# Performance work log

Hardware: AMD Instinct MI355X
Metric: run time of the kernel (lower is better)

Reference implementation:

```python
import jax, jax.numpy as jnp
import numpy as np
import math

SQRT2 = float(np.sqrt(2.0))
INV_SQRT_2PI = float(1.0 / np.sqrt(2.0 * np.pi))


def _trunc_prob(x, mu, sigma):
    # Faithful port of TruncNormal.prob with a=-10, b=10
    a, b = -10.0, 10.0
    phi_b = 0.5 * (1.0 + jax.scipy.special.erf((b - mu) / sigma / SQRT2))
    phi_a = 0.5 * (1.0 + jax.scipy.special.erf((a - mu) / sigma / SQRT2))
    xs = jnp.where(x > b, x + 100.0, x)
    xs = jnp.where(xs < a, xs - 100.0, xs)
    xn = (xs - mu) / sigma
    dens = jnp.exp(-0.5 * xn * xn) * INV_SQRT_2PI
    dens = jnp.where((xn > b) | (xn < a), 0.0, dens)
    return dens / (phi_b - phi_a) + 1e-10


def _S_single(zg, tt, Wx, bx, Wt, bt, Wt2, bt2, Wf, bf, Wo, bo):
    # One tiny MLP applied to one group-slice zg (shape [g]) at scalar time tt.
    g = Wx.shape[0]
    x = jnp.tanh(Wx @ zg + bx)
    half = g // 2
    freqs = jnp.exp(jnp.arange(half, dtype=zg.dtype) * (-math.log(10000.0) / half))
    te = tt * freqs
    temb = jnp.concatenate([jnp.sin(te), jnp.cos(te)])  # [g]
    tv = jax.nn.gelu(Wt @ temb + bt, approximate=False)  # torch nn.GELU (exact)
    tv = Wt2 @ tv + bt2
    h = jnp.tanh(Wf @ (x + tv) + bf)
    return jnp.tanh(Wo @ h + bo)[0]  # scalar S


def _derivs(zg, tt, Wx, bx, Wt, bt, Wt2, bt2, Wf, bf, Wo, bo):
    p = (Wx, bx, Wt, bt, Wt2, bt2, Wf, bf, Wo, bo)
    f = lambda z_, t_: _S_single(z_, t_, *p)
    S = f(zg, tt)
    s_z = jax.grad(f, 0)(zg, tt)                    # dS/dz         [g]
    H = jax.jacfwd(jax.grad(f, 0), 0)(zg, tt)       # H[j,k]=d2S/dzj dzk  [g,g]
    dSdt = jax.grad(f, 1)(zg, tt)                   # dS/dt scalar
    return S, s_z, H, dSdt


def reference(z, time_step, mu, sigma, Wx, bx, Wt, bt, Wt2, bt2, Wf, bf, Wo, bo, beta):
    G, g = Wx.shape[0], Wx.shape[1]
    B = z.shape[0]
    tt = time_step[0]

    sig2 = sigma ** 2 + 1e-5
    nlp = -(z - mu) / sig2                                   # nabla_log_phi [B,n_in]
    dlp = -1.0 / sig2                                        # delta_log_phi (scalar-ish)
    dpp = ((z - mu) ** 2 - sigma ** 2) / (sigma ** 4 + 1e-5)  # delta_phi_over_phi
    rho = _trunc_prob(z, mu, sigma)

    to_g = lambda a: a.reshape(B, G, g).transpose(1, 0, 2)   # [G,B,g]
    zr, nlp_r, dpp_r, rho_r = to_g(z), to_g(nlp), to_g(dpp), to_g(rho)

    over_b = jax.vmap(_derivs, in_axes=(0, None) + (None,) * 10)
    over_g = jax.vmap(over_b, in_axes=(0, None) + (0,) * 10)
    S, s_z, H, dSdt = over_g(zr, tt, Wx, bx, Wt, bt, Wt2, bt2, Wf, bf, Wo, bo)
    # S [G,B], s_z [G,B,g], H [G,B,g,g], dSdt [G,B]

    bb = beta.reshape(G, 1, 1)
    u = S[..., None] - bb * jnp.log(jnp.prod(rho_r, axis=2, keepdims=True))  # [G,B,1]
    u_z = s_z - bb * nlp_r                                                    # [G,B,g]
    # torch grad(S.sum(), t): t is a single shared (1,1) tensor -> gradient sums over batch
    dSdt_sum = dSdt.sum(axis=1).reshape(G, 1, 1)
    # grad((rho*u_z).sum(), z_temp): rho and nabla_log_phi are constants wrt z_temp,
    # so gradient = sum_j rho_j * H[j,k]
    corr = jnp.einsum('gbj,gbjk->gbk', rho_r, H)
    u_t = dSdt_sum + bb * corr / (rho_r + 1e-5)
    # grad(s_z.sum(), z_temp)[k] = sum_j H[j,k]
    u_zz = H.sum(axis=2) - bb * dlp
    pde = u_t + 0.5 * u_z ** 2 + 0.125 * bb ** 2 * (nlp_r ** 2 - 2.0 * dpp_r)

    to_bn = lambda a: a.transpose(1, 0, 2).reshape(B, -1)
    return to_bn(pde), to_bn(u_z), u[:, :, 0].transpose(1, 0), to_bn(u_zz)


def setup_inputs() -> dict:
    B, N_IN, g = 8192, 512, 4
    G = N_IN // g
    key = jax.random.key(0)
    ks = jax.random.split(key, 16)

    def lin_w(k, fo, fi):
        return (jax.random.normal(k, (G, fo, fi), jnp.float32) / np.sqrt(fi)).astype(jnp.float32)

    def lin_b(k, fo):
        return (0.01 * jax.random.normal(k, (G, fo), jnp.float32)).astype(jnp.float32)

    return {
        "z": jax.random.normal(ks[0], (B, N_IN), jnp.float32),
        "time_step": jnp.ones((1,), jnp.float32),
        "mu": jnp.zeros((1,), jnp.float32),
        "sigma": jnp.ones((1,), jnp.float32),
        "Wx": lin_w(ks[1], g, g), "bx": lin_b(ks[2], g),
        "Wt": lin_w(ks[3], g, g), "bt": lin_b(ks[4], g),
        "Wt2": lin_w(ks[5], g, g), "bt2": lin_b(ks[6], g),
        "Wf": lin_w(ks[7], g, g), "bf": lin_b(ks[8], g),
        "Wo": lin_w(ks[9], 1, g), "bo": lin_b(ks[10], 1),
        "beta": jnp.ones((G, 1), jnp.float32),
    }
```

## Files before the change

### kernel.cpp

```cpp
#include <hip/hip_runtime.h>
#include <math.h>

#define NG 128
#define NIN 512
#define OFF1 4194304
#define OFF2 8388608
#define OFF3 9437184

#define INV_SQRT_2PI 0.3989422804014327f
#define INV_SQRT2    0.7071067811865476f

typedef float f32x4 __attribute__((ext_vector_type(4)));

__device__ __forceinline__ float ftanh(float x){
    float e = __expf(2.0f*x);
    float r = __builtin_amdgcn_rcpf(e + 1.0f);
    return 1.0f - 2.0f*r;
}
__device__ __forceinline__ float frcp(float x){ return __builtin_amdgcn_rcpf(x); }

__device__ __forceinline__ float gelu_f(float x){
    return 0.5f*x*(1.0f + erff(x*INV_SQRT2));
}
__device__ __forceinline__ float gelu_df(float x){
    return 0.5f*(1.0f + erff(x*INV_SQRT2)) + x*INV_SQRT_2PI*__expf(-0.5f*x*x);
}

__global__ void k_pre(const float* __restrict__ ts,
                      const float* __restrict__ mup, const float* __restrict__ sigp,
                      const float* __restrict__ Wt,  const float* __restrict__ bt,
                      const float* __restrict__ Wt2, const float* __restrict__ bt2,
                      float* __restrict__ tv_ws, float* __restrict__ dtv_ws,
                      float* __restrict__ consts){
    int g = threadIdx.x;
    if (g == 0){
        float mu = mup[0], sigma = sigp[0];
        float sig2   = sigma*sigma + 1e-5f;
        float phi_b  = 0.5f*(1.0f+erff((10.0f-mu)/sigma*INV_SQRT2));
        float phi_a  = 0.5f*(1.0f+erff((-10.0f-mu)/sigma*INV_SQRT2));
        consts[0] = sig2;
        consts[1] = -1.0f/sig2;
        consts[2] = 1.0f/(sigma*sigma*sigma*sigma + 1e-5f);
        consts[3] = 1.0f/(phi_b-phi_a);
        consts[4] = mu;
        consts[5] = 1.0f/sigma;
        consts[6] = sigma;
    }
    if (g >= NG) return;
    float t  = ts[0];
    const float f1 = 0.01f;
    float s0, c0, s1, c1;
    __sincosf(t, &s0, &c0);
    __sincosf(t*f1, &s1, &c1);
    float temb[4]  = { s0, s1, c0, c1 };
    float dtemb[4] = { c0, f1*c1, -s0, -f1*s1 };
    float tg[4], dg[4];
    #pragma unroll
    for (int i=0;i<4;i++){
        float a = bt[g*4+i], d = 0.0f;
        #pragma unroll
        for (int j=0;j<4;j++){
            float w = Wt[g*16+i*4+j];
            a += w*temb[j]; d += w*dtemb[j];
        }
        tg[i] = gelu_f(a);
        dg[i] = gelu_df(a)*d;
    }
    #pragma unroll
    for (int j=0;j<4;j++){
        float a = bt2[g*4+j], d = 0.0f;
        #pragma unroll
        for (int i=0;i<4;i++){
            float w = Wt2[g*16+j*4+i];
            a += w*tg[i]; d += w*dg[i];
        }
        tv_ws[g*4+j]  = a;
        dtv_ws[g*4+j] = d;
    }
}

__global__ __launch_bounds__(256) void k_main(const float* __restrict__ z,
    const float* __restrict__ Wx, const float* __restrict__ bx,
    const float* __restrict__ Wf, const float* __restrict__ bf,
    const float* __restrict__ Wo, const float* __restrict__ bo,
    const float* __restrict__ betap, const float* __restrict__ tv_ws,
    const float* __restrict__ dtv_ws, const float* __restrict__ consts,
    float* __restrict__ partial, float* __restrict__ out){
    const int tid  = threadIdx.x;
    const int gidx = tid & 127;
    const int b    = blockIdx.x*2 + (tid>>7);

    const float sig2    = consts[0];
    const float dlp     = consts[1];
    const float inv_s4  = consts[2];
    const float invZ    = consts[3];
    const float mu      = consts[4];
    const float inv_sig = consts[5];
    const float sigma   = consts[6];
    const float inv_sig2 = frcp(sig2);

    float wx[16], wf[16];
    #pragma unroll
    for (int i=0;i<4;i++){
        float4 a4 = ((const float4*)(Wx + gidx*16))[i];
        wx[i*4+0]=a4.x; wx[i*4+1]=a4.y; wx[i*4+2]=a4.z; wx[i*4+3]=a4.w;
        float4 b4 = ((const float4*)(Wf + gidx*16))[i];
        wf[i*4+0]=b4.x; wf[i*4+1]=b4.y; wf[i*4+2]=b4.z; wf[i*4+3]=b4.w;
    }
    float4 t4;
    t4 = ((const float4*)bx)[gidx];     float bxA[4]={t4.x,t4.y,t4.z,t4.w};
    t4 = ((const float4*)bf)[gidx];     float bfA[4]={t4.x,t4.y,t4.z,t4.w};
    t4 = ((const float4*)Wo)[gidx];     float w3[4] ={t4.x,t4.y,t4.z,t4.w};
    t4 = ((const float4*)tv_ws)[gidx];  float tvA[4]={t4.x,t4.y,t4.z,t4.w};
    t4 = ((const float4*)dtv_ws)[gidx]; float dtvA[4]={t4.x,t4.y,t4.z,t4.w};
    const float bo0 = bo[gidx];
    const float bb  = betap[gidx];

    float4 zv = *((const float4*)(z + b*NIN + gidx*4));
    float zz[4]={zv.x,zv.y,zv.z,zv.w};

    float x[4], xp[4], u1[4];
    #pragma unroll
    for (int i=0;i<4;i++){
        float a = bxA[i] + wx[i*4]*zz[0]+wx[i*4+1]*zz[1]+wx[i*4+2]*zz[2]+wx[i*4+3]*zz[3];
        x[i] = ftanh(a); xp[i] = 1.0f - x[i]*x[i];
        u1[i] = x[i] + tvA[i];
    }
    float h[4], hp[4];
    float a3 = bo0;
    #pragma unroll
    for (int i=0;i<4;i++){
        float a = bfA[i] + wf[i*4]*u1[0]+wf[i*4+1]*u1[1]+wf[i*4+2]*u1[2]+wf[i*4+3]*u1[3];
        h[i] = ftanh(a); hp[i] = 1.0f - h[i]*h[i];
        a3 += w3[i]*h[i];
    }
    float S = ftanh(a3), sp = 1.0f - S*S;

    float Bm[16];
    #pragma unroll
    for (int i=0;i<4;i++){
        #pragma unroll
        for (int n=0;n<4;n++){
            float s = 0.0f;
            #pragma unroll
            for (int k=0;k<4;k++) s += wf[i*4+k]*xp[k]*wx[k*4+n];
            Bm[i*4+n]=s;
        }
    }
    float w3hp[4], v[4];
    #pragma unroll
    for (int i=0;i<4;i++){ w3hp[i]=w3[i]*hp[i]; v[i]=sp*w3hp[i]; }
    float q[4]={0.f,0.f,0.f,0.f};
    #pragma unroll
    for (int i=0;i<4;i++){
        #pragma unroll
        for (int j=0;j<4;j++) q[j] += v[i]*wf[i*4+j];
    }
    float dsdt_acc = q[0]*dtvA[0]+q[1]*dtvA[1]+q[2]*dtvA[2]+q[3]*dtvA[3];

    float c[4];
    #pragma unroll
    for (int n=0;n<4;n++){
        float s=0.0f;
        #pragma unroll
        for (int i=0;i<4;i++) s += w3hp[i]*Bm[i*4+n];
        c[n]=s;
    }
    const float alpha = -2.0f*S*sp;
    float bet[4], gam[4];
    #pragma unroll
    for (int i=0;i<4;i++){ bet[i] = -2.0f*h[i]*v[i]; gam[i] = -2.0f*x[i]*xp[i]*q[i]; }

    float rho[4], nlp[4], dpp[4];
    #pragma unroll
    for (int j=0;j<4;j++){
        float zj = zz[j];
        float xs = zj > 10.0f ? zj+100.0f : zj;
        xs = xs < -10.0f ? xs-100.0f : xs;
        float xn = (xs-mu)*inv_sig;
        float dens = __expf(-0.5f*xn*xn)*INV_SQRT_2PI;
        dens = (xn > 10.0f || xn < -10.0f) ? 0.0f : dens;
        rho[j] = dens*invZ + 1e-10f;
        nlp[j] = -(zj-mu)*inv_sig2;
        float d = zj-mu;
        dpp[j] = (d*d - sigma*sigma)*inv_s4;
    }
    float u_val = S - bb*__logf(rho[0]*rho[1]*rho[2]*rho[3]);

    float rc=0.0f, scs=0.0f;
    #pragma unroll
    for (int j=0;j<4;j++){ rc += rho[j]*c[j]; scs += c[j]; }
    float rB[4], sB[4], rA[4], sA[4];
    #pragma unroll
    for (int i=0;i<4;i++){
        float r1=0.0f, s=0.0f, r2=0.0f, s2=0.0f;
        #pragma unroll
        for (int j=0;j<4;j++){
            r1 += rho[j]*Bm[i*4+j]; s  += Bm[i*4+j];
            r2 += rho[j]*wx[i*4+j]; s2 += wx[i*4+j];
        }
        rB[i]=r1; sB[i]=s; rA[i]=r2; sA[i]=s2;
    }

    float pde[4], uz[4], uzz[4];
    #pragma unroll
    for (int k=0;k<4;k++){
        float corr = alpha*rc*c[k];
        float hsum = alpha*scs*c[k];
        #pragma unroll
        for (int i=0;i<4;i++){
            corr += bet[i]*rB[i]*Bm[i*4+k];
            hsum += bet[i]*sB[i]*Bm[i*4+k];
            corr += gam[i]*rA[i]*wx[i*4+k];
            hsum += gam[i]*sA[i]*wx[i*4+k];
        }
        float uzk = sp*c[k] - bb*nlp[k];
        uz[k]  = uzk;
        uzz[k] = hsum - bb*dlp;
        pde[k] = bb*corr*frcp(rho[k]+1e-5f)
               + 0.5f*uzk*uzk + 0.125f*bb*bb*(nlp[k]*nlp[k] - 2.0f*dpp[k]);
    }

    const int base = b*NIN + gidx*4;
    *((float4*)(out + base)) = make_float4(pde[0],pde[1],pde[2],pde[3]);
    f32x4 uzv  = { uz[0],  uz[1],  uz[2],  uz[3]  };
    f32x4 uzzv = { uzz[0], uzz[1], uzz[2], uzz[3] };
    __builtin_nontemporal_store(uzv,  (f32x4*)(out + OFF1 + base));
    __builtin_nontemporal_store(u_val, out + OFF2 + b*NG + gidx);
    __builtin_nontemporal_store(uzzv, (f32x4*)(out + OFF3 + base));

    __shared__ float sred[256];
    sred[tid] = dsdt_acc;
    __syncthreads();
    if (tid < 128) partial[blockIdx.x*128 + tid] = sred[tid] + sred[tid+128];
}

__global__ __launch_bounds__(256) void k_red(const float* __restrict__ partial,
                                             float* __restrict__ dsum){
    int g = blockIdx.x;
    int tid = threadIdx.x;
    float a = 0.0f;
    for (int i=tid;i<4096;i+=256) a += partial[i*128+g];
    __shared__ float s[256];
    s[tid] = a;
    __syncthreads();
    if (tid < 64){
        a = s[tid] + s[tid+64] + s[tid+128] + s[tid+192];
        #pragma unroll
        for (int o=32;o>0;o>>=1) a += __shfl_down(a, o);
        if (tid==0) dsum[g] = a;
    }
}

__global__ __launch_bounds__(256) void k_fix(const float* __restrict__ dsum,
                                             float* __restrict__ out){
    const int idx = blockIdx.x*256 + threadIdx.x;
    const float ds = dsum[threadIdx.x & 127];
    float4* p = ((float4*)out) + idx;
    float4 v = *p;
    v.x += ds; v.y += ds; v.z += ds; v.w += ds;
    *p = v;
}

extern "C" void kernel_launch(void* const* d_in, const int* in_sizes, int n_in,
                              void* d_out, int out_size, void* d_ws, size_t ws_size,
                              hipStream_t stream){
    (void)in_sizes; (void)n_in; (void)out_size; (void)ws_size;
    const float* z     = (const float*)d_in[0];
    const float* ts    = (const float*)d_in[1];
    const float* mu    = (const float*)d_in[2];
    const float* sigma = (const float*)d_in[3];
    const float* Wx    = (const float*)d_in[4];
    const float* bx    = (const float*)d_in[5];
    const float* Wt    = (const float*)d_in[6];
    const float* bt    = (const float*)d_in[7];
    const float* Wt2   = (const float*)d_in[8];
    const float* bt2   = (const float*)d_in[9];
    const float* Wf    = (const float*)d_in[10];
    const float* bf    = (const float*)d_in[11];
    const float* Wo    = (const float*)d_in[12];
    const float* bo    = (const float*)d_in[13];
    const float* beta  = (const float*)d_in[14];
    float* out = (float*)d_out;

    float* ws      = (float*)d_ws;
    float* tv_ws   = ws;
    float* dtv_ws  = ws + 512;
    float* consts  = ws + 1024;
    float* dsum    = ws + 1032;
    float* partial = ws + 1160;

    k_pre <<<1,   128, 0, stream>>>(ts, mu, sigma, Wt, bt, Wt2, bt2, tv_ws, dtv_ws, consts);
    k_main<<<4096,256, 0, stream>>>(z, Wx, bx, Wf, bf, Wo, bo, beta, tv_ws, dtv_ws,
                                    consts, partial, out);
    k_red <<<128, 256, 0, stream>>>(partial, dsum);
    k_fix <<<4096,256, 0, stream>>>(dsum, out);
}
```

Baseline: 129.5 us.

## Process two rows per thread and replace partial-sum reduction kernel with atomics

Each thread now handles two batch rows, which halves the grid and amortizes the per-thread weight loads across twice the work. The dS/dt partial sums are accumulated with atomicAdd into dsum (zeroed in k_pre), so the separate k_red launch and the partial buffer are gone. Launch bounds now request 3 blocks per SM. The trade-offs are higher register pressure from the two-row arrays, 128 contended atomic addresses hit by 2048 blocks, and a non-deterministic summation order.

```diff
diff --git a/kernel.cpp b/kernel.cpp
--- a/kernel.cpp
+++ b/kernel.cpp
@@ -31,13 +31,14 @@
                       const float* __restrict__ Wt,  const float* __restrict__ bt,
                       const float* __restrict__ Wt2, const float* __restrict__ bt2,
                       float* __restrict__ tv_ws, float* __restrict__ dtv_ws,
-                      float* __restrict__ consts){
+                      float* __restrict__ consts, float* __restrict__ dsum){
     int g = threadIdx.x;
+    if (g < NG) dsum[g] = 0.0f;
     if (g == 0){
         float mu = mup[0], sigma = sigp[0];
-        float sig2   = sigma*sigma + 1e-5f;
-        float phi_b  = 0.5f*(1.0f+erff((10.0f-mu)/sigma*INV_SQRT2));
-        float phi_a  = 0.5f*(1.0f+erff((-10.0f-mu)/sigma*INV_SQRT2));
+        float sig2  = sigma*sigma + 1e-5f;
+        float phi_b = 0.5f*(1.0f+erff((10.0f-mu)/sigma*INV_SQRT2));
+        float phi_a = 0.5f*(1.0f+erff((-10.0f-mu)/sigma*INV_SQRT2));
         consts[0] = sig2;
         consts[1] = -1.0f/sig2;
         consts[2] = 1.0f/(sigma*sigma*sigma*sigma + 1e-5f);
@@ -79,16 +80,16 @@
     }
 }
 
-__global__ __launch_bounds__(256) void k_main(const float* __restrict__ z,
+__global__ __launch_bounds__(256, 3) void k_main(const float* __restrict__ z,
     const float* __restrict__ Wx, const float* __restrict__ bx,
     const float* __restrict__ Wf, const float* __restrict__ bf,
     const float* __restrict__ Wo, const float* __restrict__ bo,
     const float* __restrict__ betap, const float* __restrict__ tv_ws,
     const float* __restrict__ dtv_ws, const float* __restrict__ consts,
-    float* __restrict__ partial, float* __restrict__ out){
+    float* __restrict__ dsum, float* __restrict__ out){
     const int tid  = threadIdx.x;
     const int gidx = tid & 127;
-    const int b    = blockIdx.x*2 + (tid>>7);
+    const int row0 = blockIdx.x*4 + (tid>>7)*2;
 
     const float sig2    = consts[0];
     const float dlp     = consts[1];
@@ -116,139 +117,159 @@
     const float bo0 = bo[gidx];
     const float bb  = betap[gidx];
 
-    float4 zv = *((const float4*)(z + b*NIN + gidx*4));
-    float zz[4]={zv.x,zv.y,zv.z,zv.w};
-
-    float x[4], xp[4], u1[4];
-    #pragma unroll
-    for (int i=0;i<4;i++){
-        float a = bxA[i] + wx[i*4]*zz[0]+wx[i*4+1]*zz[1]+wx[i*4+2]*zz[2]+wx[i*4+3]*zz[3];
-        x[i] = ftanh(a); xp[i] = 1.0f - x[i]*x[i];
-        u1[i] = x[i] + tvA[i];
-    }
-    float h[4], hp[4];
-    float a3 = bo0;
-    #pragma unroll
-    for (int i=0;i<4;i++){
-        float a = bfA[i] + wf[i*4]*u1[0]+wf[i*4+1]*u1[1]+wf[i*4+2]*u1[2]+wf[i*4+3]*u1[3];
-        h[i] = ftanh(a); hp[i] = 1.0f - h[i]*h[i];
-        a3 += w3[i]*h[i];
-    }
-    float S = ftanh(a3), sp = 1.0f - S*S;
-
-    float Bm[16];
-    #pragma unroll
-    for (int i=0;i<4;i++){
+    float zz[2][4], x_[2][4], xp[2][4], h_[2][4], hp[2][4], S[2], sp[2], q[2][4];
+    #pragma unroll
+    for (int r=0;r<2;r++){
+        float4 zv = *((const float4*)(z + (row0+r)*NIN + gidx*4));
+        zz[r][0]=zv.x; zz[r][1]=zv.y; zz[r][2]=zv.z; zz[r][3]=zv.w;
+    }
+    float u1[2][4];
+    #pragma unroll
+    for (int r=0;r<2;r++){
+        #pragma unroll
+        for (int i=0;i<4;i++){
+            float a = bxA[i] + wx[i*4]*zz[r][0]+wx[i*4+1]*zz[r][1]
+                             + wx[i*4+2]*zz[r][2]+wx[i*4+3]*zz[r][3];
+            x_[r][i] = ftanh(a);
+        }
+    }
+    #pragma unroll
+    for (int r=0;r<2;r++){
+        #pragma unroll
+        for (int i=0;i<4;i++){
+            xp[r][i] = 1.0f - x_[r][i]*x_[r][i];
+            u1[r][i] = x_[r][i] + tvA[i];
+        }
+    }
+    float a3[2] = { bo0, bo0 };
+    #pragma unroll
+    for (int r=0;r<2;r++){
+        #pragma unroll
+        for (int i=0;i<4;i++){
+            float a = bfA[i] + wf[i*4]*u1[r][0]+wf[i*4+1]*u1[r][1]
+                             + wf[i*4+2]*u1[r][2]+wf[i*4+3]*u1[r][3];
+            h_[r][i] = ftanh(a);
+        }
+    }
+    #pragma unroll
+    for (int r=0;r<2;r++){
+        #pragma unroll
+        for (int i=0;i<4;i++){
+            hp[r][i] = 1.0f - h_[r][i]*h_[r][i];
+            a3[r] += w3[i]*h_[r][i];
+        }
+    }
+    #pragma unroll
+    for (int r=0;r<2;r++){ S[r] = ftanh(a3[r]); sp[r] = 1.0f - S[r]*S[r]; }
+    #pragma unroll
+    for (int r=0;r<2;r++){
+        q[r][0]=q[r][1]=q[r][2]=q[r][3]=0.0f;
+        #pragma unroll
+        for (int i=0;i<4;i++){
+            float vi = sp[r]*w3[i]*hp[r][i];
+            #pragma unroll
+            for (int j=0;j<4;j++) q[r][j] += vi*wf[i*4+j];
+        }
+    }
+
+    {
+        float acc = (q[0][0]+q[1][0])*dtvA[0] + (q[0][1]+q[1][1])*dtvA[1]
+                  + (q[0][2]+q[1][2])*dtvA[2] + (q[0][3]+q[1][3])*dtvA[3];
+        __shared__ float sred[256];
+        sred[tid] = acc;
+        __syncthreads();
+        if (tid < 128) atomicAdd(&dsum[tid], sred[tid] + sred[tid+128]);
+    }
+
+    #pragma unroll
+    for (int r=0;r<2;r++){
+        float Bm[16];
+        #pragma unroll
+        for (int i=0;i<4;i++){
+            #pragma unroll
+            for (int n=0;n<4;n++){
+                float s = 0.0f;
+                #pragma unroll
+                for (int k=0;k<4;k++) s += wf[i*4+k]*xp[r][k]*wx[k*4+n];
+                Bm[i*4+n]=s;
+            }
+        }
+        float w3hp[4], v[4];
+        #pragma unroll
+        for (int i=0;i<4;i++){ w3hp[i]=w3[i]*hp[r][i]; v[i]=sp[r]*w3hp[i]; }
+        float c[4];
         #pragma unroll
         for (int n=0;n<4;n++){
-            float s = 0.0f;
-            #pragma unroll
-            for (int k=0;k<4;k++) s += wf[i*4+k]*xp[k]*wx[k*4+n];
-            Bm[i*4+n]=s;
-        }
-    }
-    float w3hp[4], v[4];
-    #pragma unroll
-    for (int i=0;i<4;i++){ w3hp[i]=w3[i]*hp[i]; v[i]=sp*w3hp[i]; }
-    float q[4]={0.f,0.f,0.f,0.f};
-    #pragma unroll
-    for (int i=0;i<4;i++){
-        #pragma unroll
-        for (int j=0;j<4;j++) q[j] += v[i]*wf[i*4+j];
-    }
-    float dsdt_acc = q[0]*dtvA[0]+q[1]*dtvA[1]+q[2]*dtvA[2]+q[3]*dtvA[3];
-
-    float c[4];
-    #pragma unroll
-    for (int n=0;n<4;n++){
-        float s=0.0f;
-        #pragma unroll
-        for (int i=0;i<4;i++) s += w3hp[i]*Bm[i*4+n];
-        c[n]=s;
-    }
-    const float alpha = -2.0f*S*sp;
-    float bet[4], gam[4];
-    #pragma unroll
-    for (int i=0;i<4;i++){ bet[i] = -2.0f*h[i]*v[i]; gam[i] = -2.0f*x[i]*xp[i]*q[i]; }
-
-    float rho[4], nlp[4], dpp[4];
-    #pragma unroll
-    for (int j=0;j<4;j++){
-        float zj = zz[j];
-        float xs = zj > 10.0f ? zj+100.0f : zj;
-        xs = xs < -10.0f ? xs-100.0f : xs;
-        float xn = (xs-mu)*inv_sig;
-        float dens = __expf(-0.5f*xn*xn)*INV_SQRT_2PI;
-        dens = (xn > 10.0f || xn < -10.0f) ? 0.0f : dens;
-        rho[j] = dens*invZ + 1e-10f;
-        nlp[j] = -(zj-mu)*inv_sig2;
-        float d = zj-mu;
-        dpp[j] = (d*d - sigma*sigma)*inv_s4;
-    }
-    float u_val = S - bb*__logf(rho[0]*rho[1]*rho[2]*rho[3]);
-
-    float rc=0.0f, scs=0.0f;
-    #pragma unroll
-    for (int j=0;j<4;j++){ rc += rho[j]*c[j]; scs += c[j]; }
-    float rB[4], sB[4], rA[4], sA[4];
-    #pragma unroll
-    for (int i=0;i<4;i++){
-        float r1=0.0f, s=0.0f, r2=0.0f, s2=0.0f;
+            float s=0.0f;
+            #pragma unroll
+            for (int i=0;i<4;i++) s += w3hp[i]*Bm[i*4+n];
+            c[n]=s;
+        }
+        const float alpha = -2.0f*S[r]*sp[r];
+        float bet[4], gam[4];
+        #pragma unroll
+        for (int i=0;i<4;i++){
+            bet[i] = -2.0f*h_[r][i]*v[i];
+            gam[i] = -2.0f*x_[r][i]*xp[r][i]*q[r][i];
+        }
+
+        float rho[4], nlp[4], dpp[4];
         #pragma unroll
         for (int j=0;j<4;j++){
-            r1 += rho[j]*Bm[i*4+j]; s  += Bm[i*4+j];
-            r2 += rho[j]*wx[i*4+j]; s2 += wx[i*4+j];
-        }
-        rB[i]=r1; sB[i]=s; rA[i]=r2; sA[i]=s2;
-    }
-
-    float pde[4], uz[4], uzz[4];
-    #pragma unroll
-    for (int k=0;k<4;k++){
-        float corr = alpha*rc*c[k];
-        float hsum = alpha*scs*c[k];
-        #pragma unroll
-        for (int i=0;i<4;i++){
-            corr += bet[i]*rB[i]*Bm[i*4+k];
-            hsum += bet[i]*sB[i]*Bm[i*4+k];
-            corr += gam[i]*rA[i]*wx[i*4+k];
-            hsum += gam[i]*sA[i]*wx[i*4+k];
-        }
-        float uzk = sp*c[k] - bb*nlp[k];
-        uz[k]  = uzk;
-        uzz[k] = hsum - bb*dlp;
-        pde[k] = bb*corr*frcp(rho[k]+1e-5f)
-               + 0.5f*uzk*uzk + 0.125f*bb*bb*(nlp[k]*nlp[k] - 2.0f*dpp[k]);
-    }
-
-    const int base = b*NIN + gidx*4;
-    *((float4*)(out + base)) = make_float4(pde[0],pde[1],pde[2],pde[3]);
-    f32x4 uzv  = { uz[0],  uz[1],  uz[2],  uz[3]  };
-    f32x4 uzzv = { uzz[0], uzz[1], uzz[2], uzz[3] };
-    __builtin_nontemporal_store(uzv,  (f32x4*)(out + OFF1 + base));
-    __builtin_nontemporal_store(u_val, out + OFF2 + b*NG + gidx);
-    __builtin_nontemporal_store(uzzv, (f32x4*)(out + OFF3 + base));
-
-    __shared__ float sred[256];
-    sred[tid] = dsdt_acc;
-    __syncthreads();
-    if (tid < 128) partial[blockIdx.x*128 + tid] = sred[tid] + sred[tid+128];
-}
-
-__global__ __launch_bounds__(256) void k_red(const float* __restrict__ partial,
-                                             float* __restrict__ dsum){
-    int g = blockIdx.x;
-    int tid = threadIdx.x;
-    float a = 0.0f;
-    for (int i=tid;i<4096;i+=256) a += partial[i*128+g];
-    __shared__ float s[256];
-    s[tid] = a;
-    __syncthreads();
-    if (tid < 64){
-        a = s[tid] + s[tid+64] + s[tid+128] + s[tid+192];
-        #pragma unroll
-        for (int o=32;o>0;o>>=1) a += __shfl_down(a, o);
-        if (tid==0) dsum[g] = a;
+            float zj = zz[r][j];
+            float xs = zj > 10.0f ? zj+100.0f : zj;
+            xs = xs < -10.0f ? xs-100.0f : xs;
+            float xn = (xs-mu)*inv_sig;
+            float dens = __expf(-0.5f*xn*xn)*INV_SQRT_2PI;
+            dens = (xn > 10.0f || xn < -10.0f) ? 0.0f : dens;
+            rho[j] = dens*invZ + 1e-10f;
+            nlp[j] = -(zj-mu)*inv_sig2;
+            float d = zj-mu;
+            dpp[j] = (d*d - sigma*sigma)*inv_s4;
+        }
+        float u_val = S[r] - bb*__logf(rho[0]*rho[1]*rho[2]*rho[3]);
+
+        float rc=0.0f, scs=0.0f;
+        #pragma unroll
+        for (int j=0;j<4;j++){ rc += rho[j]*c[j]; scs += c[j]; }
+        float rB[4], sB[4], rA[4], sA[4];
+        #pragma unroll
+        for (int i=0;i<4;i++){
+            float r1=0.0f, s=0.0f, r2=0.0f, s2=0.0f;
+            #pragma unroll
+            for (int j=0;j<4;j++){
+                r1 += rho[j]*Bm[i*4+j]; s  += Bm[i*4+j];
+                r2 += rho[j]*wx[i*4+j]; s2 += wx[i*4+j];
+            }
+            rB[i]=r1; sB[i]=s; rA[i]=r2; sA[i]=s2;
+        }
+
+        float pde[4], uz[4], uzz[4];
+        #pragma unroll
+        for (int k=0;k<4;k++){
+            float corr = alpha*rc*c[k];
+            float hsum = alpha*scs*c[k];
+            #pragma unroll
+            for (int i=0;i<4;i++){
+                corr += bet[i]*rB[i]*Bm[i*4+k];
+                hsum += bet[i]*sB[i]*Bm[i*4+k];
+                corr += gam[i]*rA[i]*wx[i*4+k];
+                hsum += gam[i]*sA[i]*wx[i*4+k];
+            }
+            float uzk = sp[r]*c[k] - bb*nlp[k];
+            uz[k]  = uzk;
+            uzz[k] = hsum - bb*dlp;
+            pde[k] = bb*corr*frcp(rho[k]+1e-5f)
+                   + 0.5f*uzk*uzk + 0.125f*bb*bb*(nlp[k]*nlp[k] - 2.0f*dpp[k]);
+        }
+
+        const int base = (row0+r)*NIN + gidx*4;
+        *((float4*)(out + base)) = make_float4(pde[0],pde[1],pde[2],pde[3]);
+        f32x4 uzv  = { uz[0],  uz[1],  uz[2],  uz[3]  };
+        f32x4 uzzv = { uzz[0], uzz[1], uzz[2], uzz[3] };
+        __builtin_nontemporal_store(uzv,  (f32x4*)(out + OFF1 + base));
+        __builtin_nontemporal_store(u_val, out + OFF2 + (row0+r)*NG + gidx);
+        __builtin_nontemporal_store(uzzv, (f32x4*)(out + OFF3 + base));
     }
 }
 
@@ -288,11 +309,10 @@
     float* dtv_ws  = ws + 512;
     float* consts  = ws + 1024;
     float* dsum    = ws + 1032;
-    float* partial = ws + 1160;
-
-    k_pre <<<1,   128, 0, stream>>>(ts, mu, sigma, Wt, bt, Wt2, bt2, tv_ws, dtv_ws, consts);
-    k_main<<<4096,256, 0, stream>>>(z, Wx, bx, Wf, bf, Wo, bo, beta, tv_ws, dtv_ws,
-                                    consts, partial, out);
-    k_red <<<128, 256, 0, stream>>>(partial, dsum);
+
+    k_pre <<<1,   128, 0, stream>>>(ts, mu, sigma, Wt, bt, Wt2, bt2,
+                                    tv_ws, dtv_ws, consts, dsum);
+    k_main<<<2048,256, 0, stream>>>(z, Wx, bx, Wf, bf, Wo, bo, beta, tv_ws,
+                                    dtv_ws, consts, dsum, out);
     k_fix <<<4096,256, 0, stream>>>(dsum, out);
 }
```

After: 176.5 us. 1.36x slower.
